# Optimization experiments

Hardware: AMD Instinct MI355X
Metric: run time of the kernel (lower is better)

The kernel has to match this reference:

```python
import jax, jax.numpy as jnp
import numpy as np

HID = 150

def _lstm_layer(x, Wih, Whh, bih, bhh):
    # x: [T, D] -> [T, HID]; PyTorch gate order i, f, g, o
    b = bih + bhh
    xg = x @ Wih.T + b  # precompute input contribution: [T, 4H]
    def step(carry, xg_t):
        h, c = carry
        g = xg_t + h @ Whh.T
        i, f, gg, o = jnp.split(g, 4)
        i = jax.nn.sigmoid(i); f = jax.nn.sigmoid(f)
        gg = jnp.tanh(gg); o = jax.nn.sigmoid(o)
        c = f * c + i * gg
        h = o * jnp.tanh(c)
        return (h, c), h
    init = (jnp.zeros((HID,), x.dtype), jnp.zeros((HID,), x.dtype))
    _, ys = jax.lax.scan(step, init, xg)
    return ys

def _bilstm(x, Wih, Whh, bih, bhh):
    # x: [T, D]; params stacked [L, 2, ...]
    out = x
    for l in range(Wih.shape[0]):
        fwd = _lstm_layer(out, Wih[l, 0], Whh[l, 0], bih[l, 0], bhh[l, 0])
        bwd = _lstm_layer(out[::-1], Wih[l, 1], Whh[l, 1], bih[l, 1], bhh[l, 1])[::-1]
        out = jnp.concatenate([fwd, bwd], axis=-1)  # [T, 2H]
    return out

def setup_inputs() -> dict:
    key = jax.random.key(0)
    ks = jax.random.split(key, 16)
    s = 0.1  # keep LSTM gates in a sane range
    return {
        "inputs_solv": jax.random.normal(ks[0], (1, 4096, 300), jnp.float32),
        "inputs_solu": jax.random.normal(ks[1], (1, 4096, 300), jnp.float32),
        "solv_Wih": jax.random.normal(ks[2], (2, 2, 600, 300), jnp.float32) * s,
        "solv_Whh": jax.random.normal(ks[3], (2, 2, 600, 150), jnp.float32) * s,
        "solv_bih": jax.random.normal(ks[4], (2, 2, 600), jnp.float32) * s,
        "solv_bhh": jax.random.normal(ks[5], (2, 2, 600), jnp.float32) * s,
        "solu_Wih": jax.random.normal(ks[6], (2, 2, 600, 300), jnp.float32) * s,
        "solu_Whh": jax.random.normal(ks[7], (2, 2, 600, 150), jnp.float32) * s,
        "solu_bih": jax.random.normal(ks[8], (2, 2, 600), jnp.float32) * s,
        "solu_bhh": jax.random.normal(ks[9], (2, 2, 600), jnp.float32) * s,
        "fc1_w": jax.random.normal(ks[10], (2000, 600), jnp.float32) * 0.02,
        "fc1_b": jax.random.normal(ks[11], (2000,), jnp.float32) * 0.02,
        "fc2_w": jax.random.normal(ks[12], (1, 2000), jnp.float32) * 0.02,
        "fc2_b": jax.random.normal(ks[13], (1,), jnp.float32) * 0.02,
    }

def reference(inputs_solv, inputs_solu, solv_Wih, solv_Whh, solv_bih, solv_bhh,
              solu_Wih, solu_Whh, solu_bih, solu_bhh, fc1_w, fc1_b, fc2_w, fc2_b):
    H = _bilstm(inputs_solv[0], solv_Wih, solv_Whh, solv_bih, solv_bhh)  # [Hs, 300]
    G = _bilstm(inputs_solu[0], solu_Wih, solu_Whh, solu_bih, solu_bhh)  # [Gs, 300]
    a_score = H @ G.T                      # fused version of the nested loop: [Hs, Gs]
    a = jax.nn.softmax(a_score, axis=1)
    P = a @ G                              # [Hs, 300]
    Q = a.T @ H                            # [Gs, 300]
    u = jnp.maximum(H, P)
    v = jnp.maximum(G, Q)
    inp = jnp.concatenate([u.sum(axis=0), v.sum(axis=0)], axis=0)  # [600]
    x = jax.nn.relu(inp @ fc1_w.T + fc1_b)
    return x @ fc2_w.T + fc2_b
```

## Files before the change

### kernel.cpp

```cpp
#include <hip/hip_runtime.h>
#include <hip/hip_fp16.h>
#include <cstddef>

#define T_LEN 4096
#define HID 150
#define G4 600
#define NC 300

typedef __attribute__((ext_vector_type(8))) short bf16x8;
typedef __attribute__((ext_vector_type(8))) _Float16 f16x8;
typedef __attribute__((ext_vector_type(4))) float f32x4;

__device__ __forceinline__ void barrier_lgkm() {
  asm volatile("s_waitcnt lgkmcnt(0)\n\ts_barrier" ::: "memory");
}

__device__ __forceinline__ float fsig(float x) {
  return __builtin_amdgcn_rcpf(1.f + __expf(-x));
}
__device__ __forceinline__ float ftanh(float x) {
  float ax = fabsf(x);
  float e = __expf(2.f * ax);
  float t = 1.f - 2.f * __builtin_amdgcn_rcpf(e + 1.f);
  return copysignf(t, x);
}
__device__ __forceinline__ unsigned short f2bf(float f) {
  unsigned u = __builtin_bit_cast(unsigned, f);
  u += 0x7fff + ((u >> 16) & 1);
  return (unsigned short)(u >> 16);
}

__global__ __launch_bounds__(512, 2) void lstm_scan(
    const float* __restrict__ whh_solv, const float* __restrict__ whh_solu,
    const float* __restrict__ xg_base,
    float* __restrict__ out_solv, float* __restrict__ out_solu, int layer)
{
  __shared__ __align__(16) unsigned short h_bf[160];
  __shared__ float g_s[640];
  const int c = blockIdx.x;
  const int net = c >> 1, dir = c & 1;
  const float* Whh = (net ? whh_solu : whh_solv) + (size_t)(layer * 2 + dir) * (G4 * HID);
  const float* xg = xg_base + (size_t)c * T_LEN * G4;
  float* out = (net ? out_solu : out_solv) + dir * HID;
  const int tid = threadIdx.x;
  const int lane = tid & 63, wv = tid >> 6;
  const int lrow = lane & 15, lq = lane >> 4;

  bf16x8 bfr[5][5];
#pragma unroll
  for (int j = 0; j < 5; j++) {
    const int jrow = 16 * (wv + 8 * j) + lrow;
#pragma unroll
    for (int kk = 0; kk < 5; kk++) {
      bf16x8 b;
#pragma unroll
      for (int i = 0; i < 8; i++) {
        const int k = kk * 32 + lq * 8 + i;
        const float v = (jrow < G4 && k < HID) ? Whh[(size_t)jrow * HID + k] : 0.f;
        b[i] = (short)f2bf(v);
      }
      bfr[j][kk] = b;
    }
  }
  if (tid < 160) h_bf[tid] = 0;
  float cst = 0.f;
  float xr0 = 0.f, xr1 = 0.f, xr2 = 0.f, xr3 = 0.f;
  if (tid < HID) {
    const int t0 = dir ? (T_LEN - 1) : 0;
    const float* xgr = xg + (size_t)t0 * G4 + tid;
    xr0 = xgr[0]; xr1 = xgr[HID]; xr2 = xgr[2 * HID]; xr3 = xgr[3 * HID];
  }
  bf16x8 af[5];
#pragma unroll
  for (int kk = 0; kk < 5; kk++) af[kk] = (bf16x8){0, 0, 0, 0, 0, 0, 0, 0};
  const f32x4 z4 = {0.f, 0.f, 0.f, 0.f};
  barrier_lgkm();

  for (int s = 0; s < T_LEN; s++) {
    const int t = dir ? (T_LEN - 1 - s) : s;
    if (lrow == 0) {
#pragma unroll
      for (int kk = 0; kk < 5; kk++) af[kk] = *(const bf16x8*)&h_bf[kk * 32 + lq * 8];
    }
    f32x4 acc[5];
#pragma unroll
    for (int j = 0; j < 5; j++)
      acc[j] = __builtin_amdgcn_mfma_f32_16x16x32_bf16(af[0], bfr[j][0], z4, 0, 0, 0);
#pragma unroll
    for (int kk = 1; kk < 5; kk++)
#pragma unroll
      for (int j = 0; j < 5; j++)
        acc[j] = __builtin_amdgcn_mfma_f32_16x16x32_bf16(af[kk], bfr[j][kk], acc[j], 0, 0, 0);
    if (lane < 16) {
#pragma unroll
      for (int j = 0; j < 5; j++) g_s[16 * (wv + 8 * j) + lane] = acc[j][0];
    }
    barrier_lgkm();
    if (tid < HID) {
      const int n = tid;
      float gi = xr0 + g_s[n];
      float gf = xr1 + g_s[HID + n];
      float gg = xr2 + g_s[2 * HID + n];
      float go = xr3 + g_s[3 * HID + n];
      if (s + 1 < T_LEN) {
        const int tn = dir ? (T_LEN - 2 - s) : (s + 1);
        const float* xgr = xg + (size_t)tn * G4 + n;
        xr0 = xgr[0]; xr1 = xgr[HID]; xr2 = xgr[2 * HID]; xr3 = xgr[3 * HID];
      }
      const float iv = fsig(gi), fv = fsig(gf), gv = ftanh(gg), ov = fsig(go);
      cst = fv * cst + iv * gv;
      const float hv = ov * ftanh(cst);
      h_bf[n] = f2bf(hv);
      out[(size_t)t * NC + n] = hv;
    }
    barrier_lgkm();
  }
}

__global__ void conv_w(const float* __restrict__ wv, const float* __restrict__ wu,
                       __half* __restrict__ dst)
{
  const int gid = blockIdx.x * 256 + threadIdx.x;
  if (gid >= 8 * 640 * 320) return;
  const int k = gid % 320, j = (gid / 320) % 640, s = gid / (320 * 640);
  const int l = s >> 2, net = (s >> 1) & 1, dir = s & 1;
  float v = 0.f;
  if (j < G4 && k < NC) {
    const float* src = (net ? wu : wv) + (size_t)(l * 2 + dir) * (G4 * NC);
    v = src[(size_t)j * NC + k];
  }
  dst[gid] = __float2half(v);
}

__global__ void conv_x(const float* __restrict__ src, __half* __restrict__ dst, int rows)
{
  const int gid = blockIdx.x * 256 + threadIdx.x;
  if (gid >= rows * 320) return;
  const int k = gid % 320, m = gid / 320;
  dst[gid] = __float2half(k < NC ? src[(size_t)m * NC + k] : 0.f);
}

__global__ void conv_t(const float* __restrict__ src, __half* __restrict__ dst)
{
  const int gid = blockIdx.x * 256 + threadIdx.x;
  if (gid >= 320 * 4096) return;
  const int m = gid % 4096, f = gid / 4096;
  dst[gid] = __float2half(f < NC ? src[(size_t)m * NC + f] : 0.f);
}

__global__ void zero_f(float* __restrict__ p, int n) {
  const int i = blockIdx.x * 256 + threadIdx.x;
  if (i < n) p[i] = 0.f;
}

__global__ __launch_bounds__(256) void xg_mfma(
    const __half* __restrict__ Av, const __half* __restrict__ Au,
    const __half* __restrict__ W,
    const float* __restrict__ bihv, const float* __restrict__ bhhv,
    const float* __restrict__ bihu, const float* __restrict__ bhhu,
    float* __restrict__ xg, int layer)
{
  const int tid = threadIdx.x;
  const int lane = tid & 63, wv = tid >> 6;
  const int ln = lane & 15, q = lane >> 4;
  const int chain = blockIdx.y;
  const __half* A = (chain >= 2) ? Au : Av;
  const __half* Wc = W + (size_t)chain * 640 * 320;
  const float* bi = ((chain >= 2) ? bihu : bihv) + (size_t)(layer * 2 + (chain & 1)) * G4;
  const float* bh = ((chain >= 2) ? bhhu : bhhv) + (size_t)(layer * 2 + (chain & 1)) * G4;
  float* C = xg + (size_t)chain * T_LEN * G4;
  const int m0 = blockIdx.x * 64 + wv * 16;
  const __half* Arow = A + (size_t)(m0 + ln) * 320;

  for (int nc = 0; nc < 4; nc++) {
    f32x4 acc[10];
#pragma unroll
    for (int j = 0; j < 10; j++) acc[j] = (f32x4){0.f, 0.f, 0.f, 0.f};
    for (int kk = 0; kk < 10; kk++) {
      const f16x8 afr = *(const f16x8*)(Arow + kk * 32 + q * 8);
#pragma unroll
      for (int j = 0; j < 10; j++) {
        const int n = nc * 160 + j * 16 + ln;
        const f16x8 bfr = *(const f16x8*)(Wc + (size_t)n * 320 + kk * 32 + q * 8);
        acc[j] = __builtin_amdgcn_mfma_f32_16x16x32_f16(afr, bfr, acc[j], 0, 0, 0);
      }
    }
#pragma unroll
    for (int j = 0; j < 10; j++) {
      const int n = nc * 160 + j * 16 + ln;
      if (n < G4) {
        const float bias = bi[n] + bh[n];
#pragma unroll
        for (int r = 0; r < 4; r++)
          C[(size_t)(m0 + q * 4 + r) * G4 + n] = acc[j][r] + bias;
      }
    }
  }
}

__global__ __launch_bounds__(256) void s_pass1(
    const __half* __restrict__ Hh, const __half* __restrict__ Gh,
    float* __restrict__ sums)
{
  const int tid = threadIdx.x;
  const int lane = tid & 63, wv = tid >> 6;
  const int ln = lane & 15, q = lane >> 4;
  const int m0 = blockIdx.x * 64 + wv * 16;
  const __half* Arow = Hh + (size_t)(m0 + ln) * 320;
  f16x8 afr[10];
#pragma unroll
  for (int kk = 0; kk < 10; kk++) afr[kk] = *(const f16x8*)(Arow + kk * 32 + q * 8);
  float rs[4] = {0.f, 0.f, 0.f, 0.f};
  const int nt0 = blockIdx.y * 64;
  for (int nt = 0; nt < 64; nt++) {
    const __half* Brow = Gh + (size_t)(16 * (nt0 + nt) + ln) * 320;
    f32x4 acc = (f32x4){0.f, 0.f, 0.f, 0.f};
#pragma unroll
    for (int kk = 0; kk < 10; kk++) {
      const f16x8 bfr = *(const f16x8*)(Brow + kk * 32 + q * 8);
      acc = __builtin_amdgcn_mfma_f32_16x16x32_f16(afr[kk], bfr, acc, 0, 0, 0);
    }
#pragma unroll
    for (int r = 0; r < 4; r++) rs[r] += __expf(fminf(acc[r] - 30.f, 80.f));
  }
#pragma unroll
  for (int m = 1; m <= 8; m <<= 1)
#pragma unroll
    for (int r = 0; r < 4; r++) rs[r] += __shfl_xor(rs[r], m);
  if (ln == 0) {
#pragma unroll
    for (int r = 0; r < 4; r++) atomicAdd(&sums[m0 + q * 4 + r], rs[r]);
  }
}

__global__ void invert_k(const float* __restrict__ sums, float* __restrict__ il) {
  const int i = blockIdx.x * 256 + threadIdx.x;
  if (i < 4096) il[i] = 1.f / sums[i];
}

__global__ __launch_bounds__(256) void s_pass2(
    const __half* __restrict__ Hh, const __half* __restrict__ Gh,
    const float* __restrict__ il, __half* __restrict__ AH)
{
  const int tid = threadIdx.x;
  const int lane = tid & 63, wv = tid >> 6;
  const int ln = lane & 15, q = lane >> 4;
  const int m0 = blockIdx.x * 64 + wv * 16;
  const __half* Arow = Hh + (size_t)(m0 + ln) * 320;
  f16x8 afr[10];
#pragma unroll
  for (int kk = 0; kk < 10; kk++) afr[kk] = *(const f16x8*)(Arow + kk * 32 + q * 8);
  float ilr[4];
#pragma unroll
  for (int r = 0; r < 4; r++) ilr[r] = il[m0 + q * 4 + r];
  const int nt0 = blockIdx.y * 64;
  for (int nt = 0; nt < 64; nt++) {
    const int n = 16 * (nt0 + nt) + ln;
    const __half* Brow = Gh + (size_t)n * 320;
    f32x4 acc = (f32x4){0.f, 0.f, 0.f, 0.f};
#pragma unroll
    for (int kk = 0; kk < 10; kk++) {
      const f16x8 bfr = *(const f16x8*)(Brow + kk * 32 + q * 8);
      acc = __builtin_amdgcn_mfma_f32_16x16x32_f16(afr[kk], bfr, acc, 0, 0, 0);
    }
#pragma unroll
    for (int r = 0; r < 4; r++) {
      const float a = __expf(fminf(acc[r] - 30.f, 80.f)) * ilr[r];
      AH[(size_t)(m0 + q * 4 + r) * 4096 + n] = __float2half(a);
    }
  }
}

__global__ __launch_bounds__(256) void p_mfma(
    const __half* __restrict__ AH, const __half* __restrict__ GhT,
    float* __restrict__ Pb)
{
  const int tid = threadIdx.x;
  const int lane = tid & 63, wv = tid >> 6;
  const int ln = lane & 15, q = lane >> 4;
  const int m0 = blockIdx.x * 64 + wv * 16;
  const __half* Arow = AH + (size_t)(m0 + ln) * 4096;

  for (int nc = 0; nc < 2; nc++) {
    f32x4 acc[10];
#pragma unroll
    for (int j = 0; j < 10; j++) acc[j] = (f32x4){0.f, 0.f, 0.f, 0.f};
    for (int kk = 0; kk < 128; kk++) {
      const f16x8 afr = *(const f16x8*)(Arow + kk * 32 + q * 8);
#pragma unroll
      for (int j = 0; j < 10; j++) {
        const int n = nc * 160 + j * 16 + ln;
        const f16x8 bfr = *(const f16x8*)(GhT + (size_t)n * 4096 + kk * 32 + q * 8);
        acc[j] = __builtin_amdgcn_mfma_f32_16x16x32_f16(afr, bfr, acc[j], 0, 0, 0);
      }
    }
#pragma unroll
    for (int j = 0; j < 10; j++) {
      const int n = nc * 160 + j * 16 + ln;
      if (n < NC) {
#pragma unroll
        for (int r = 0; r < 4; r++)
          Pb[(size_t)(m0 + q * 4 + r) * NC + n] = acc[j][r];
      }
    }
  }
}

__global__ __launch_bounds__(256) void qt_mfma(
    const __half* __restrict__ AH, const __half* __restrict__ HhT,
    float* __restrict__ Qb)
{
  __shared__ __align__(16) _Float16 Ats[64][72];
  const int tid = threadIdx.x;
  const int lane = tid & 63, wv = tid >> 6;
  const int ln = lane & 15, q = lane >> 4;
  const int j0 = blockIdx.x * 64;
  f32x4 acc[20];
#pragma unroll
  for (int j = 0; j < 20; j++) acc[j] = (f32x4){0.f, 0.f, 0.f, 0.f};
  const int il8 = tid >> 2, j8 = (tid & 3) * 16;

  for (int ic = 0; ic < 4096; ic += 64) {
    __syncthreads();
    {
      const __half* src = AH + (size_t)(ic + il8) * 4096 + j0 + j8;
      const f16x8 v0 = *(const f16x8*)src;
      const f16x8 v1 = *(const f16x8*)(src + 8);
#pragma unroll
      for (int jj = 0; jj < 8; jj++) Ats[j8 + jj][il8] = v0[jj];
#pragma unroll
      for (int jj = 0; jj < 8; jj++) Ats[j8 + 8 + jj][il8] = v1[jj];
    }
    __syncthreads();
#pragma unroll
    for (int s = 0; s < 2; s++) {
      const f16x8 afr = *(const f16x8*)&Ats[wv * 16 + ln][s * 32 + q * 8];
      const __half* bbase = HhT + ic + s * 32 + q * 8;
#pragma unroll
      for (int j = 0; j < 20; j++) {
        const f16x8 bfr = *(const f16x8*)(bbase + (size_t)(j * 16 + ln) * 4096);
        acc[j] = __builtin_amdgcn_mfma_f32_16x16x32_f16(afr, bfr, acc[j], 0, 0, 0);
      }
    }
  }
#pragma unroll
  for (int j = 0; j < 20; j++) {
    const int f = j * 16 + ln;
    if (f < NC) {
#pragma unroll
      for (int r = 0; r < 4; r++)
        Qb[(size_t)(j0 + wv * 16 + q * 4 + r) * NC + f] = acc[j][r];
    }
  }
}

__global__ void reduce_uv(const float* __restrict__ X, const float* __restrict__ Yp,
                          float* __restrict__ inp, int off)
{
  const int j = threadIdx.x;
  if (j >= NC) return;
  const int r0 = blockIdx.x * 128;
  float s = 0.f;
  for (int r = r0; r < r0 + 128; r++)
    s += fmaxf(X[(size_t)r * NC + j], Yp[(size_t)r * NC + j]);
  atomicAdd(&inp[off + j], s);
}

__global__ void fc1_k(const float* __restrict__ w1, const float* __restrict__ b1,
                      const float* __restrict__ inp, float* __restrict__ x)
{
  const int r = blockIdx.x * 256 + threadIdx.x;
  if (r >= 2000) return;
  float s = b1[r];
  const float* wr = w1 + (size_t)r * 600;
  for (int k = 0; k < 600; k++) s += wr[k] * inp[k];
  x[r] = fmaxf(s, 0.f);
}

__global__ void fc2_k(const float* __restrict__ x, const float* __restrict__ w2,
                      const float* __restrict__ b2, float* __restrict__ outp)
{
  const int tid = threadIdx.x;
  float s = 0.f;
  for (int i = tid; i < 2000; i += 256) s += x[i] * w2[i];
#pragma unroll
  for (int off = 32; off > 0; off >>= 1) s += __shfl_down(s, off);
  __shared__ float red[4];
  if ((tid & 63) == 0) red[tid >> 6] = s;
  __syncthreads();
  if (tid == 0) outp[0] = red[0] + red[1] + red[2] + red[3] + b2[0];
}

extern "C" void kernel_launch(void* const* d_in, const int* in_sizes, int n_in,
                              void* d_out, int out_size, void* d_ws, size_t ws_size,
                              hipStream_t stream)
{
  const float* in_solv  = (const float*)d_in[0];
  const float* in_solu  = (const float*)d_in[1];
  const float* solv_Wih = (const float*)d_in[2];
  const float* solv_Whh = (const float*)d_in[3];
  const float* solv_bih = (const float*)d_in[4];
  const float* solv_bhh = (const float*)d_in[5];
  const float* solu_Wih = (const float*)d_in[6];
  const float* solu_Whh = (const float*)d_in[7];
  const float* solu_bih = (const float*)d_in[8];
  const float* solu_bhh = (const float*)d_in[9];
  const float* fc1_w = (const float*)d_in[10];
  const float* fc1_b = (const float*)d_in[11];
  const float* fc2_w = (const float*)d_in[12];
  const float* fc2_b = (const float*)d_in[13];
  float* outp = (float*)d_out;
  float* ws = (float*)d_ws;

  constexpr size_t off_P   = 0;
  constexpr size_t off_Q   = 1228800;
  constexpr size_t off_inp = 2457600;
  constexpr size_t off_x   = 2458240;
  constexpr size_t off_il  = 2460288;
  constexpr size_t off_sm  = 2464384;
  constexpr size_t off_xg  = 2468480;
  constexpr size_t off_L0  = off_xg + (size_t)4 * 2457600;
  constexpr size_t off_HG  = off_L0 + (size_t)2 * 1228800;

  float*  xg   = ws + off_xg;
  float*  L0v  = ws + off_L0;
  float*  L0u  = L0v + 1228800;
  float*  Hb   = ws + off_HG;
  float*  Gb   = Hb + 1228800;
  float*  Pb   = ws + off_P;
  float*  Qb   = ws + off_Q;
  float*  inp  = ws + off_inp;
  float*  xf   = ws + off_x;
  float*  il   = ws + off_il;
  float*  sums = ws + off_sm;
  __half* Wihh = (__half*)(ws + off_P);
  __half* Avh  = (__half*)(ws + off_L0);
  __half* Auh  = Avh + 4096 * 320;
  __half* L0vh = (__half*)(ws + off_HG);
  __half* L0uh = L0vh + 4096 * 320;
  __half* Hh   = (__half*)(ws + off_L0);
  __half* Gh   = Hh + 4096 * 320;
  __half* AH   = (__half*)(ws + off_xg);
  __half* HhT  = AH + (size_t)4096 * 4096;
  __half* GhT  = HhT + 320 * 4096;

  conv_w<<<(8 * 640 * 320 + 255) / 256, 256, 0, stream>>>(solv_Wih, solu_Wih, Wihh);
  conv_x<<<(4096 * 320 + 255) / 256, 256, 0, stream>>>(in_solv, Avh, 4096);
  conv_x<<<(4096 * 320 + 255) / 256, 256, 0, stream>>>(in_solu, Auh, 4096);

  xg_mfma<<<dim3(64, 4), 256, 0, stream>>>(Avh, Auh, Wihh,
      solv_bih, solv_bhh, solu_bih, solu_bhh, xg, 0);
  lstm_scan<<<4, 512, 0, stream>>>(solv_Whh, solu_Whh, xg, L0v, L0u, 0);

  conv_x<<<(4096 * 320 + 255) / 256, 256, 0, stream>>>(L0v, L0vh, 4096);
  conv_x<<<(4096 * 320 + 255) / 256, 256, 0, stream>>>(L0u, L0uh, 4096);
  xg_mfma<<<dim3(64, 4), 256, 0, stream>>>(L0vh, L0uh, Wihh + (size_t)4 * 640 * 320,
      solv_bih, solv_bhh, solu_bih, solu_bhh, xg, 1);
  lstm_scan<<<4, 512, 0, stream>>>(solv_Whh, solu_Whh, xg, Hb, Gb, 1);

  conv_x<<<(4096 * 320 + 255) / 256, 256, 0, stream>>>(Hb, Hh, 4096);
  conv_x<<<(4096 * 320 + 255) / 256, 256, 0, stream>>>(Gb, Gh, 4096);
  conv_t<<<(320 * 4096 + 255) / 256, 256, 0, stream>>>(Hb, HhT);
  conv_t<<<(320 * 4096 + 255) / 256, 256, 0, stream>>>(Gb, GhT);
  zero_f<<<16, 256, 0, stream>>>(sums, 4096);
  s_pass1<<<dim3(64, 4), 256, 0, stream>>>(Hh, Gh, sums);
  invert_k<<<16, 256, 0, stream>>>(sums, il);
  s_pass2<<<dim3(64, 4), 256, 0, stream>>>(Hh, Gh, il, AH);
  p_mfma<<<64, 256, 0, stream>>>(AH, GhT, Pb);
  qt_mfma<<<64, 256, 0, stream>>>(AH, HhT, Qb);

  zero_f<<<3, 256, 0, stream>>>(inp, 640);
  reduce_uv<<<32, 320, 0, stream>>>(Hb, Pb, inp, 0);
  reduce_uv<<<32, 320, 0, stream>>>(Gb, Qb, inp, 300);
  fc1_k<<<8, 256, 0, stream>>>(fc1_w, fc1_b, inp, xf);
  fc2_k<<<1, 256, 0, stream>>>(xf, fc2_w, fc2_b, outp);
}
```

Measured before the change: 7.672 ms.

## Remap LSTM gate rows per wave to drop shared-memory gate exchange and a barrier

Recurrent weight rows are reassigned so that each wave's MFMA tiles produce all four gates for its own hidden units. Waves 0-7 cover units 0-127, and a fifth tile, run only by waves 0-5, carries units 128-149 with interleaved gates gathered by lane shuffles. This removes the g_s shared buffer and one of the two block barriers in each of the 4096 serial timesteps, and skips the padded MFMAs on the last two waves. The cost is that nothing separates one wave's read of h_bf from another wave's write of the new h within the same step, so correctness relies on timing rather than a barrier.

```diff
diff --git a/kernel.cpp b/kernel.cpp
--- a/kernel.cpp
+++ b/kernel.cpp
@@ -36,7 +36,6 @@
     float* __restrict__ out_solv, float* __restrict__ out_solu, int layer)
 {
   __shared__ __align__(16) unsigned short h_bf[160];
-  __shared__ float g_s[640];
   const int c = blockIdx.x;
   const int net = c >> 1, dir = c & 1;
   const float* Whh = (net ? whh_solu : whh_solv) + (size_t)(layer * 2 + dir) * (G4 * HID);
@@ -44,31 +43,40 @@
   float* out = (net ? out_solu : out_solv) + dir * HID;
   const int tid = threadIdx.x;
   const int lane = tid & 63, wv = tid >> 6;
-  const int lrow = lane & 15, lq = lane >> 4;
+  const int l = lane & 15, q = lane >> 4;
+  const int u = 16 * wv + l;
+  const bool gate_lane = (lane < 16);
+  const bool sec_lane = gate_lane && ((l & 3) == 0) && (u < 88);
+  const int cp = u;
+  const int cs = 128 + (u >> 2);
 
   bf16x8 bfr[5][5];
 #pragma unroll
   for (int j = 0; j < 5; j++) {
-    const int jrow = 16 * (wv + 8 * j) + lrow;
+    int row;
+    if (j < 4) row = j * HID + u;
+    else       row = (u < 88) ? (u & 3) * HID + 128 + (u >> 2) : -1;
 #pragma unroll
     for (int kk = 0; kk < 5; kk++) {
       bf16x8 b;
 #pragma unroll
       for (int i = 0; i < 8; i++) {
-        const int k = kk * 32 + lq * 8 + i;
-        const float v = (jrow < G4 && k < HID) ? Whh[(size_t)jrow * HID + k] : 0.f;
+        const int k = kk * 32 + q * 8 + i;
+        const float v = (row >= 0 && k < HID) ? Whh[(size_t)row * HID + k] : 0.f;
         b[i] = (short)f2bf(v);
       }
       bfr[j][kk] = b;
     }
   }
   if (tid < 160) h_bf[tid] = 0;
-  float cst = 0.f;
-  float xr0 = 0.f, xr1 = 0.f, xr2 = 0.f, xr3 = 0.f;
-  if (tid < HID) {
+  float cstp = 0.f, csts = 0.f;
+  float xp0 = 0.f, xp1 = 0.f, xp2 = 0.f, xp3 = 0.f;
+  float xs0 = 0.f, xs1 = 0.f, xs2 = 0.f, xs3 = 0.f;
+  {
     const int t0 = dir ? (T_LEN - 1) : 0;
-    const float* xgr = xg + (size_t)t0 * G4 + tid;
-    xr0 = xgr[0]; xr1 = xgr[HID]; xr2 = xgr[2 * HID]; xr3 = xgr[3 * HID];
+    const float* base = xg + (size_t)t0 * G4;
+    if (gate_lane) { xp0 = base[cp]; xp1 = base[HID + cp]; xp2 = base[2 * HID + cp]; xp3 = base[3 * HID + cp]; }
+    if (sec_lane)  { xs0 = base[cs]; xs1 = base[HID + cs]; xs2 = base[2 * HID + cs]; xs3 = base[3 * HID + cs]; }
   }
   bf16x8 af[5];
 #pragma unroll
@@ -78,40 +86,48 @@
 
   for (int s = 0; s < T_LEN; s++) {
     const int t = dir ? (T_LEN - 1 - s) : s;
-    if (lrow == 0) {
-#pragma unroll
-      for (int kk = 0; kk < 5; kk++) af[kk] = *(const bf16x8*)&h_bf[kk * 32 + lq * 8];
+    if (l == 0) {
+#pragma unroll
+      for (int kk = 0; kk < 5; kk++) af[kk] = *(const bf16x8*)&h_bf[kk * 32 + q * 8];
     }
     f32x4 acc[5];
 #pragma unroll
-    for (int j = 0; j < 5; j++)
+    for (int j = 0; j < 4; j++)
       acc[j] = __builtin_amdgcn_mfma_f32_16x16x32_bf16(af[0], bfr[j][0], z4, 0, 0, 0);
-#pragma unroll
-    for (int kk = 1; kk < 5; kk++)
-#pragma unroll
-      for (int j = 0; j < 5; j++)
+    if (wv < 6)
+      acc[4] = __builtin_amdgcn_mfma_f32_16x16x32_bf16(af[0], bfr[4][0], z4, 0, 0, 0);
+#pragma unroll
+    for (int kk = 1; kk < 5; kk++) {
+#pragma unroll
+      for (int j = 0; j < 4; j++)
         acc[j] = __builtin_amdgcn_mfma_f32_16x16x32_bf16(af[kk], bfr[j][kk], acc[j], 0, 0, 0);
-    if (lane < 16) {
-#pragma unroll
-      for (int j = 0; j < 5; j++) g_s[16 * (wv + 8 * j) + lane] = acc[j][0];
-    }
-    barrier_lgkm();
-    if (tid < HID) {
-      const int n = tid;
-      float gi = xr0 + g_s[n];
-      float gf = xr1 + g_s[HID + n];
-      float gg = xr2 + g_s[2 * HID + n];
-      float go = xr3 + g_s[3 * HID + n];
+      if (wv < 6)
+        acc[4] = __builtin_amdgcn_mfma_f32_16x16x32_bf16(af[kk], bfr[4][kk], acc[4], 0, 0, 0);
+    }
+    if (gate_lane) {
+      const float g4 = acc[4][0];
+      const int b4 = lane & ~3;
+      const float v0 = __shfl(g4, b4), v1 = __shfl(g4, b4 | 1);
+      const float v2 = __shfl(g4, b4 | 2), v3 = __shfl(g4, b4 | 3);
+      if (sec_lane) {
+        const float si = xs0 + v0, sf = xs1 + v1, sg = xs2 + v2, so = xs3 + v3;
+        csts = fsig(sf) * csts + fsig(si) * ftanh(sg);
+        const float hs = fsig(so) * ftanh(csts);
+        h_bf[cs] = f2bf(hs);
+        out[(size_t)t * NC + cs] = hs;
+      }
+      const float gi = xp0 + acc[0][0], gf = xp1 + acc[1][0];
+      const float gg = xp2 + acc[2][0], go = xp3 + acc[3][0];
+      cstp = fsig(gf) * cstp + fsig(gi) * ftanh(gg);
+      const float hp = fsig(go) * ftanh(cstp);
+      h_bf[cp] = f2bf(hp);
+      out[(size_t)t * NC + cp] = hp;
       if (s + 1 < T_LEN) {
         const int tn = dir ? (T_LEN - 2 - s) : (s + 1);
-        const float* xgr = xg + (size_t)tn * G4 + n;
-        xr0 = xgr[0]; xr1 = xgr[HID]; xr2 = xgr[2 * HID]; xr3 = xgr[3 * HID];
-      }
-      const float iv = fsig(gi), fv = fsig(gf), gv = ftanh(gg), ov = fsig(go);
-      cst = fv * cst + iv * gv;
-      const float hv = ov * ftanh(cst);
-      h_bf[n] = f2bf(hv);
-      out[(size_t)t * NC + n] = hv;
+        const float* base = xg + (size_t)tn * G4;
+        xp0 = base[cp]; xp1 = base[HID + cp]; xp2 = base[2 * HID + cp]; xp3 = base[3 * HID + cp];
+        if (sec_lane) { xs0 = base[cs]; xs1 = base[HID + cs]; xs2 = base[2 * HID + cs]; xs3 = base[3 * HID + cs]; }
+      }
     }
     barrier_lgkm();
   }
```

After: 9.483 ms. 23.6% more time.

## Regroup LSTM gate rows per wave and double-buffer h to drop a barrier

Applied to the files above, without the earlier changes.

The recurrent scan now assigns each of 10 waves the four gate rows (i,f,g,o) for the same 16 hidden units. Each wave can then compute the cell update directly from its MFMA accumulators instead of exchanging gate values through shared memory. The hidden state is double-buffered in LDS, so each timestep needs only one barrier instead of two. The cost is a larger block of 640 threads and some padded rows in the last wave.

```diff
diff --git a/kernel.cpp b/kernel.cpp
--- a/kernel.cpp
+++ b/kernel.cpp
@@ -30,13 +30,12 @@
   return (unsigned short)(u >> 16);
 }
 
-__global__ __launch_bounds__(512, 2) void lstm_scan(
+__global__ __launch_bounds__(640, 3) void lstm_scan(
     const float* __restrict__ whh_solv, const float* __restrict__ whh_solu,
     const float* __restrict__ xg_base,
     float* __restrict__ out_solv, float* __restrict__ out_solu, int layer)
 {
-  __shared__ __align__(16) unsigned short h_bf[160];
-  __shared__ float g_s[640];
+  __shared__ __align__(16) unsigned short hb[2][160];
   const int c = blockIdx.x;
   const int net = c >> 1, dir = c & 1;
   const float* Whh = (net ? whh_solu : whh_solv) + (size_t)(layer * 2 + dir) * (G4 * HID);
@@ -45,74 +44,75 @@
   const int tid = threadIdx.x;
   const int lane = tid & 63, wv = tid >> 6;
   const int lrow = lane & 15, lq = lane >> 4;
-
-  bf16x8 bfr[5][5];
-#pragma unroll
-  for (int j = 0; j < 5; j++) {
-    const int jrow = 16 * (wv + 8 * j) + lrow;
-#pragma unroll
-    for (int kk = 0; kk < 5; kk++) {
-      bf16x8 b;
-#pragma unroll
-      for (int i = 0; i < 8; i++) {
-        const int k = kk * 32 + lq * 8 + i;
-        const float v = (jrow < G4 && k < HID) ? Whh[(size_t)jrow * HID + k] : 0.f;
-        b[i] = (short)f2bf(v);
-      }
-      bfr[j][kk] = b;
-    }
-  }
-  if (tid < 160) h_bf[tid] = 0;
+  const bool gl = (lane < 16) && (16 * wv + lane < HID);
+  const int ch = 16 * wv + lane;
+
+  bf16x8 bfr[4][5];
+  {
+    const int cc = 16 * wv + lrow;
+    const bool cv = (cc < HID);
+#pragma unroll
+    for (int j = 0; j < 4; j++) {
+      const size_t row = (size_t)(j * HID + cc) * HID;
+#pragma unroll
+      for (int kk = 0; kk < 5; kk++) {
+        bf16x8 b;
+#pragma unroll
+        for (int i = 0; i < 8; i++) {
+          const int k = kk * 32 + lq * 8 + i;
+          const float v = (cv && k < HID) ? Whh[row + k] : 0.f;
+          b[i] = (short)f2bf(v);
+        }
+        bfr[j][kk] = b;
+      }
+    }
+  }
+  if (tid < 160) { hb[0][tid] = 0; hb[1][tid] = 0; }
   float cst = 0.f;
   float xr0 = 0.f, xr1 = 0.f, xr2 = 0.f, xr3 = 0.f;
-  if (tid < HID) {
+  if (gl) {
     const int t0 = dir ? (T_LEN - 1) : 0;
-    const float* xgr = xg + (size_t)t0 * G4 + tid;
+    const float* xgr = xg + (size_t)t0 * G4 + ch;
     xr0 = xgr[0]; xr1 = xgr[HID]; xr2 = xgr[2 * HID]; xr3 = xgr[3 * HID];
   }
-  bf16x8 af[5];
-#pragma unroll
-  for (int kk = 0; kk < 5; kk++) af[kk] = (bf16x8){0, 0, 0, 0, 0, 0, 0, 0};
   const f32x4 z4 = {0.f, 0.f, 0.f, 0.f};
   barrier_lgkm();
 
+  int p = 0;
   for (int s = 0; s < T_LEN; s++) {
     const int t = dir ? (T_LEN - 1 - s) : s;
-    if (lrow == 0) {
-#pragma unroll
-      for (int kk = 0; kk < 5; kk++) af[kk] = *(const bf16x8*)&h_bf[kk * 32 + lq * 8];
-    }
-    f32x4 acc[5];
-#pragma unroll
-    for (int j = 0; j < 5; j++)
+    bf16x8 af[5];
+#pragma unroll
+    for (int kk = 0; kk < 5; kk++) {
+      bf16x8 a = {0, 0, 0, 0, 0, 0, 0, 0};
+      if (lrow == 0) a = *(const bf16x8*)&hb[p][kk * 32 + lq * 8];
+      af[kk] = a;
+    }
+    f32x4 acc[4];
+#pragma unroll
+    for (int j = 0; j < 4; j++)
       acc[j] = __builtin_amdgcn_mfma_f32_16x16x32_bf16(af[0], bfr[j][0], z4, 0, 0, 0);
 #pragma unroll
     for (int kk = 1; kk < 5; kk++)
 #pragma unroll
-      for (int j = 0; j < 5; j++)
+      for (int j = 0; j < 4; j++)
         acc[j] = __builtin_amdgcn_mfma_f32_16x16x32_bf16(af[kk], bfr[j][kk], acc[j], 0, 0, 0);
-    if (lane < 16) {
-#pragma unroll
-      for (int j = 0; j < 5; j++) g_s[16 * (wv + 8 * j) + lane] = acc[j][0];
-    }
-    barrier_lgkm();
-    if (tid < HID) {
-      const int n = tid;
-      float gi = xr0 + g_s[n];
-      float gf = xr1 + g_s[HID + n];
-      float gg = xr2 + g_s[2 * HID + n];
-      float go = xr3 + g_s[3 * HID + n];
+    if (gl) {
+      const float gi = xr0 + acc[0][0];
+      const float gf = xr1 + acc[1][0];
+      const float gg = xr2 + acc[2][0];
+      const float go = xr3 + acc[3][0];
       if (s + 1 < T_LEN) {
         const int tn = dir ? (T_LEN - 2 - s) : (s + 1);
-        const float* xgr = xg + (size_t)tn * G4 + n;
+        const float* xgr = xg + (size_t)tn * G4 + ch;
         xr0 = xgr[0]; xr1 = xgr[HID]; xr2 = xgr[2 * HID]; xr3 = xgr[3 * HID];
       }
-      const float iv = fsig(gi), fv = fsig(gf), gv = ftanh(gg), ov = fsig(go);
-      cst = fv * cst + iv * gv;
-      const float hv = ov * ftanh(cst);
-      h_bf[n] = f2bf(hv);
-      out[(size_t)t * NC + n] = hv;
-    }
+      cst = fsig(gf) * cst + fsig(gi) * ftanh(gg);
+      const float hv = fsig(go) * ftanh(cst);
+      hb[1 - p][ch] = f2bf(hv);
+      out[(size_t)t * NC + ch] = hv;
+    }
+    p ^= 1;
     barrier_lgkm();
   }
 }
@@ -450,13 +450,13 @@
 
   xg_mfma<<<dim3(64, 4), 256, 0, stream>>>(Avh, Auh, Wihh,
       solv_bih, solv_bhh, solu_bih, solu_bhh, xg, 0);
-  lstm_scan<<<4, 512, 0, stream>>>(solv_Whh, solu_Whh, xg, L0v, L0u, 0);
+  lstm_scan<<<4, 640, 0, stream>>>(solv_Whh, solu_Whh, xg, L0v, L0u, 0);
 
   conv_x<<<(4096 * 320 + 255) / 256, 256, 0, stream>>>(L0v, L0vh, 4096);
   conv_x<<<(4096 * 320 + 255) / 256, 256, 0, stream>>>(L0u, L0uh, 4096);
   xg_mfma<<<dim3(64, 4), 256, 0, stream>>>(L0vh, L0uh, Wihh + (size_t)4 * 640 * 320,
       solv_bih, solv_bhh, solu_bih, solu_bhh, xg, 1);
-  lstm_scan<<<4, 512, 0, stream>>>(solv_Whh, solu_Whh, xg, Hb, Gb, 1);
+  lstm_scan<<<4, 640, 0, stream>>>(solv_Whh, solu_Whh, xg, Hb, Gb, 1);
 
   conv_x<<<(4096 * 320 + 255) / 256, 256, 0, stream>>>(Hb, Hh, 4096);
   conv_x<<<(4096 * 320 + 255) / 256, 256, 0, stream>>>(Gb, Gh, 4096);
```

Measured after the change: 7.784 ms. Within noise of the previous version (+1.5%).

## Emit fp16 LSTM outputs directly, compute attention scores once, merge P/Q GEMMs

Applied to the files above, without the earlier changes.

The LSTM scan now writes fp16 outputs straight into the padded layout the next stage reads, so the separate conv_x conversion launches go away. A zero pass over the padded buffer sets the unused columns. The two-pass softmax that recomputed H·G^T twice is replaced by one score GEMM that stores fp16 logits, followed by a row-sum kernel and an in-place exp/scale kernel. The P and Q^T GEMMs are merged into one launch of 128 blocks so they run concurrently. Storing raw logits in fp16 before the exponential adds rounding error, and the new approach reads and writes the 4096x4096 matrix several extra times.

```diff
diff --git a/kernel.cpp b/kernel.cpp
--- a/kernel.cpp
+++ b/kernel.cpp
@@ -33,7 +33,8 @@
 __global__ __launch_bounds__(512, 2) void lstm_scan(
     const float* __restrict__ whh_solv, const float* __restrict__ whh_solu,
     const float* __restrict__ xg_base,
-    float* __restrict__ out_solv, float* __restrict__ out_solu, int layer)
+    float* __restrict__ o32v, float* __restrict__ o32u,
+    __half* __restrict__ o16v, __half* __restrict__ o16u, int layer, int w32)
 {
   __shared__ __align__(16) unsigned short h_bf[160];
   __shared__ float g_s[640];
@@ -41,7 +42,8 @@
   const int net = c >> 1, dir = c & 1;
   const float* Whh = (net ? whh_solu : whh_solv) + (size_t)(layer * 2 + dir) * (G4 * HID);
   const float* xg = xg_base + (size_t)c * T_LEN * G4;
-  float* out = (net ? out_solu : out_solv) + dir * HID;
+  float* out32 = (net ? o32u : o32v) + dir * HID;
+  __half* out16 = (net ? o16u : o16v) + dir * HID;
   const int tid = threadIdx.x;
   const int lane = tid & 63, wv = tid >> 6;
   const int lrow = lane & 15, lq = lane >> 4;
@@ -70,24 +72,22 @@
     const float* xgr = xg + (size_t)t0 * G4 + tid;
     xr0 = xgr[0]; xr1 = xgr[HID]; xr2 = xgr[2 * HID]; xr3 = xgr[3 * HID];
   }
-  bf16x8 af[5];
-#pragma unroll
-  for (int kk = 0; kk < 5; kk++) af[kk] = (bf16x8){0, 0, 0, 0, 0, 0, 0, 0};
-  const f32x4 z4 = {0.f, 0.f, 0.f, 0.f};
   barrier_lgkm();
 
   for (int s = 0; s < T_LEN; s++) {
     const int t = dir ? (T_LEN - 1 - s) : s;
-    if (lrow == 0) {
-#pragma unroll
-      for (int kk = 0; kk < 5; kk++) af[kk] = *(const bf16x8*)&h_bf[kk * 32 + lq * 8];
+    bf16x8 af[5];
+#pragma unroll
+    for (int kk = 0; kk < 5; kk++) {
+      bf16x8 a = {0, 0, 0, 0, 0, 0, 0, 0};
+      if (lrow == 0) a = *(const bf16x8*)&h_bf[kk * 32 + lq * 8];
+      af[kk] = a;
     }
     f32x4 acc[5];
 #pragma unroll
-    for (int j = 0; j < 5; j++)
-      acc[j] = __builtin_amdgcn_mfma_f32_16x16x32_bf16(af[0], bfr[j][0], z4, 0, 0, 0);
-#pragma unroll
-    for (int kk = 1; kk < 5; kk++)
+    for (int j = 0; j < 5; j++) acc[j] = (f32x4){0.f, 0.f, 0.f, 0.f};
+#pragma unroll
+    for (int kk = 0; kk < 5; kk++)
 #pragma unroll
       for (int j = 0; j < 5; j++)
         acc[j] = __builtin_amdgcn_mfma_f32_16x16x32_bf16(af[kk], bfr[j][kk], acc[j], 0, 0, 0);
@@ -111,7 +111,8 @@
       cst = fv * cst + iv * gv;
       const float hv = ov * ftanh(cst);
       h_bf[n] = f2bf(hv);
-      out[(size_t)t * NC + n] = hv;
+      out16[(size_t)t * 320 + n] = __float2half(hv);
+      if (w32) out32[(size_t)t * NC + n] = hv;
     }
     barrier_lgkm();
   }
@@ -198,9 +199,9 @@
   }
 }
 
-__global__ __launch_bounds__(256) void s_pass1(
+__global__ __launch_bounds__(256) void s_gemm(
     const __half* __restrict__ Hh, const __half* __restrict__ Gh,
-    float* __restrict__ sums)
+    __half* __restrict__ AH)
 {
   const int tid = threadIdx.x;
   const int lane = tid & 63, wv = tid >> 6;
@@ -210,49 +211,6 @@
   f16x8 afr[10];
 #pragma unroll
   for (int kk = 0; kk < 10; kk++) afr[kk] = *(const f16x8*)(Arow + kk * 32 + q * 8);
-  float rs[4] = {0.f, 0.f, 0.f, 0.f};
-  const int nt0 = blockIdx.y * 64;
-  for (int nt = 0; nt < 64; nt++) {
-    const __half* Brow = Gh + (size_t)(16 * (nt0 + nt) + ln) * 320;
-    f32x4 acc = (f32x4){0.f, 0.f, 0.f, 0.f};
-#pragma unroll
-    for (int kk = 0; kk < 10; kk++) {
-      const f16x8 bfr = *(const f16x8*)(Brow + kk * 32 + q * 8);
-      acc = __builtin_amdgcn_mfma_f32_16x16x32_f16(afr[kk], bfr, acc, 0, 0, 0);
-    }
-#pragma unroll
-    for (int r = 0; r < 4; r++) rs[r] += __expf(fminf(acc[r] - 30.f, 80.f));
-  }
-#pragma unroll
-  for (int m = 1; m <= 8; m <<= 1)
-#pragma unroll
-    for (int r = 0; r < 4; r++) rs[r] += __shfl_xor(rs[r], m);
-  if (ln == 0) {
-#pragma unroll
-    for (int r = 0; r < 4; r++) atomicAdd(&sums[m0 + q * 4 + r], rs[r]);
-  }
-}
-
-__global__ void invert_k(const float* __restrict__ sums, float* __restrict__ il) {
-  const int i = blockIdx.x * 256 + threadIdx.x;
-  if (i < 4096) il[i] = 1.f / sums[i];
-}
-
-__global__ __launch_bounds__(256) void s_pass2(
-    const __half* __restrict__ Hh, const __half* __restrict__ Gh,
-    const float* __restrict__ il, __half* __restrict__ AH)
-{
-  const int tid = threadIdx.x;
-  const int lane = tid & 63, wv = tid >> 6;
-  const int ln = lane & 15, q = lane >> 4;
-  const int m0 = blockIdx.x * 64 + wv * 16;
-  const __half* Arow = Hh + (size_t)(m0 + ln) * 320;
-  f16x8 afr[10];
-#pragma unroll
-  for (int kk = 0; kk < 10; kk++) afr[kk] = *(const f16x8*)(Arow + kk * 32 + q * 8);
-  float ilr[4];
-#pragma unroll
-  for (int r = 0; r < 4; r++) ilr[r] = il[m0 + q * 4 + r];
   const int nt0 = blockIdx.y * 64;
   for (int nt = 0; nt < 64; nt++) {
     const int n = 16 * (nt0 + nt) + ln;
@@ -264,92 +222,116 @@
       acc = __builtin_amdgcn_mfma_f32_16x16x32_f16(afr[kk], bfr, acc, 0, 0, 0);
     }
 #pragma unroll
-    for (int r = 0; r < 4; r++) {
-      const float a = __expf(fminf(acc[r] - 30.f, 80.f)) * ilr[r];
-      AH[(size_t)(m0 + q * 4 + r) * 4096 + n] = __float2half(a);
-    }
-  }
-}
-
-__global__ __launch_bounds__(256) void p_mfma(
+    for (int r = 0; r < 4; r++)
+      AH[(size_t)(m0 + q * 4 + r) * 4096 + n] = __float2half(acc[r]);
+  }
+}
+
+__global__ __launch_bounds__(256) void rowsum_k(const __half* __restrict__ AH,
+                                                float* __restrict__ il)
+{
+  const int m = blockIdx.x, tid = threadIdx.x;
+  const __half* row = AH + (size_t)m * 4096;
+  float s = 0.f;
+  for (int i = tid * 8; i < 4096; i += 2048) {
+    const f16x8 v = *(const f16x8*)(row + i);
+#pragma unroll
+    for (int j = 0; j < 8; j++) s += __expf(fminf((float)v[j] - 30.f, 80.f));
+  }
+#pragma unroll
+  for (int off = 32; off > 0; off >>= 1) s += __shfl_down(s, off);
+  __shared__ float red[4];
+  if ((tid & 63) == 0) red[tid >> 6] = s;
+  __syncthreads();
+  if (tid == 0) il[m] = 1.f / (red[0] + red[1] + red[2] + red[3]);
+}
+
+__global__ __launch_bounds__(256) void scale_k(__half* __restrict__ AH,
+                                               const float* __restrict__ il)
+{
+  const size_t gid = (size_t)blockIdx.x * 256 + threadIdx.x;
+  const int m = (int)(gid >> 9);
+  const float ilm = il[m];
+  f16x8 v = *(f16x8*)(AH + gid * 8);
+#pragma unroll
+  for (int j = 0; j < 8; j++)
+    v[j] = (_Float16)(__expf(fminf((float)v[j] - 30.f, 80.f)) * ilm);
+  *(f16x8*)(AH + gid * 8) = v;
+}
+
+__global__ __launch_bounds__(256) void pq_mfma(
     const __half* __restrict__ AH, const __half* __restrict__ GhT,
-    float* __restrict__ Pb)
-{
-  const int tid = threadIdx.x;
-  const int lane = tid & 63, wv = tid >> 6;
-  const int ln = lane & 15, q = lane >> 4;
-  const int m0 = blockIdx.x * 64 + wv * 16;
-  const __half* Arow = AH + (size_t)(m0 + ln) * 4096;
-
-  for (int nc = 0; nc < 2; nc++) {
-    f32x4 acc[10];
-#pragma unroll
-    for (int j = 0; j < 10; j++) acc[j] = (f32x4){0.f, 0.f, 0.f, 0.f};
-    for (int kk = 0; kk < 128; kk++) {
-      const f16x8 afr = *(const f16x8*)(Arow + kk * 32 + q * 8);
-#pragma unroll
-      for (int j = 0; j < 10; j++) {
-        const int n = nc * 160 + j * 16 + ln;
-        const f16x8 bfr = *(const f16x8*)(GhT + (size_t)n * 4096 + kk * 32 + q * 8);
-        acc[j] = __builtin_amdgcn_mfma_f32_16x16x32_f16(afr, bfr, acc[j], 0, 0, 0);
-      }
-    }
-#pragma unroll
-    for (int j = 0; j < 10; j++) {
-      const int n = nc * 160 + j * 16 + ln;
-      if (n < NC) {
-#pragma unroll
-        for (int r = 0; r < 4; r++)
-          Pb[(size_t)(m0 + q * 4 + r) * NC + n] = acc[j][r];
-      }
-    }
-  }
-}
-
-__global__ __launch_bounds__(256) void qt_mfma(
-    const __half* __restrict__ AH, const __half* __restrict__ HhT,
-    float* __restrict__ Qb)
+    const __half* __restrict__ HhT,
+    float* __restrict__ Pb, float* __restrict__ Qb)
 {
   __shared__ __align__(16) _Float16 Ats[64][72];
   const int tid = threadIdx.x;
   const int lane = tid & 63, wv = tid >> 6;
   const int ln = lane & 15, q = lane >> 4;
-  const int j0 = blockIdx.x * 64;
-  f32x4 acc[20];
-#pragma unroll
-  for (int j = 0; j < 20; j++) acc[j] = (f32x4){0.f, 0.f, 0.f, 0.f};
-  const int il8 = tid >> 2, j8 = (tid & 3) * 16;
-
-  for (int ic = 0; ic < 4096; ic += 64) {
-    __syncthreads();
-    {
-      const __half* src = AH + (size_t)(ic + il8) * 4096 + j0 + j8;
-      const f16x8 v0 = *(const f16x8*)src;
-      const f16x8 v1 = *(const f16x8*)(src + 8);
-#pragma unroll
-      for (int jj = 0; jj < 8; jj++) Ats[j8 + jj][il8] = v0[jj];
-#pragma unroll
-      for (int jj = 0; jj < 8; jj++) Ats[j8 + 8 + jj][il8] = v1[jj];
-    }
-    __syncthreads();
-#pragma unroll
-    for (int s = 0; s < 2; s++) {
-      const f16x8 afr = *(const f16x8*)&Ats[wv * 16 + ln][s * 32 + q * 8];
-      const __half* bbase = HhT + ic + s * 32 + q * 8;
-#pragma unroll
-      for (int j = 0; j < 20; j++) {
-        const f16x8 bfr = *(const f16x8*)(bbase + (size_t)(j * 16 + ln) * 4096);
-        acc[j] = __builtin_amdgcn_mfma_f32_16x16x32_f16(afr, bfr, acc[j], 0, 0, 0);
-      }
-    }
-  }
-#pragma unroll
-  for (int j = 0; j < 20; j++) {
-    const int f = j * 16 + ln;
-    if (f < NC) {
-#pragma unroll
-      for (int r = 0; r < 4; r++)
-        Qb[(size_t)(j0 + wv * 16 + q * 4 + r) * NC + f] = acc[j][r];
+
+  if (blockIdx.x < 64) {
+    const int m0 = blockIdx.x * 64 + wv * 16;
+    const __half* Arow = AH + (size_t)(m0 + ln) * 4096;
+    for (int nc = 0; nc < 2; nc++) {
+      f32x4 acc[10];
+#pragma unroll
+      for (int j = 0; j < 10; j++) acc[j] = (f32x4){0.f, 0.f, 0.f, 0.f};
+      for (int kk = 0; kk < 128; kk++) {
+        const f16x8 afr = *(const f16x8*)(Arow + kk * 32 + q * 8);
+#pragma unroll
+        for (int j = 0; j < 10; j++) {
+          const int n = nc * 160 + j * 16 + ln;
+          const f16x8 bfr = *(const f16x8*)(GhT + (size_t)n * 4096 + kk * 32 + q * 8);
+          acc[j] = __builtin_amdgcn_mfma_f32_16x16x32_f16(afr, bfr, acc[j], 0, 0, 0);
+        }
+      }
+#pragma unroll
+      for (int j = 0; j < 10; j++) {
+        const int n = nc * 160 + j * 16 + ln;
+        if (n < NC) {
+#pragma unroll
+          for (int r = 0; r < 4; r++)
+            Pb[(size_t)(m0 + q * 4 + r) * NC + n] = acc[j][r];
+        }
+      }
+    }
+  } else {
+    const int j0 = (blockIdx.x - 64) * 64;
+    f32x4 acc[20];
+#pragma unroll
+    for (int j = 0; j < 20; j++) acc[j] = (f32x4){0.f, 0.f, 0.f, 0.f};
+    const int il8 = tid >> 2, j8 = (tid & 3) * 16;
+    for (int ic = 0; ic < 4096; ic += 64) {
+      __syncthreads();
+      {
+        const __half* src = AH + (size_t)(ic + il8) * 4096 + j0 + j8;
+        const f16x8 v0 = *(const f16x8*)src;
+        const f16x8 v1 = *(const f16x8*)(src + 8);
+#pragma unroll
+        for (int jj = 0; jj < 8; jj++) Ats[j8 + jj][il8] = v0[jj];
+#pragma unroll
+        for (int jj = 0; jj < 8; jj++) Ats[j8 + 8 + jj][il8] = v1[jj];
+      }
+      __syncthreads();
+#pragma unroll
+      for (int s = 0; s < 2; s++) {
+        const f16x8 afr = *(const f16x8*)&Ats[wv * 16 + ln][s * 32 + q * 8];
+        const __half* bbase = HhT + ic + s * 32 + q * 8;
+#pragma unroll
+        for (int j = 0; j < 20; j++) {
+          const f16x8 bfr = *(const f16x8*)(bbase + (size_t)(j * 16 + ln) * 4096);
+          acc[j] = __builtin_amdgcn_mfma_f32_16x16x32_f16(afr, bfr, acc[j], 0, 0, 0);
+        }
+      }
+    }
+#pragma unroll
+    for (int j = 0; j < 20; j++) {
+      const int f = j * 16 + ln;
+      if (f < NC) {
+#pragma unroll
+        for (int r = 0; r < 4; r++)
+          Qb[(size_t)(j0 + wv * 16 + q * 4 + r) * NC + f] = acc[j][r];
+      }
     }
   }
 }
@@ -417,14 +399,11 @@
   constexpr size_t off_inp = 2457600;
   constexpr size_t off_x   = 2458240;
   constexpr size_t off_il  = 2460288;
-  constexpr size_t off_sm  = 2464384;
   constexpr size_t off_xg  = 2468480;
   constexpr size_t off_L0  = off_xg + (size_t)4 * 2457600;
-  constexpr size_t off_HG  = off_L0 + (size_t)2 * 1228800;
+  constexpr size_t off_HG  = off_L0 + 1310720;
 
   float*  xg   = ws + off_xg;
-  float*  L0v  = ws + off_L0;
-  float*  L0u  = L0v + 1228800;
   float*  Hb   = ws + off_HG;
   float*  Gb   = Hb + 1228800;
   float*  Pb   = ws + off_P;
@@ -432,7 +411,6 @@
   float*  inp  = ws + off_inp;
   float*  xf   = ws + off_x;
   float*  il   = ws + off_il;
-  float*  sums = ws + off_sm;
   __half* Wihh = (__half*)(ws + off_P);
   __half* Avh  = (__half*)(ws + off_L0);
   __half* Auh  = Avh + 4096 * 320;
@@ -444,30 +422,27 @@
   __half* HhT  = AH + (size_t)4096 * 4096;
   __half* GhT  = HhT + 320 * 4096;
 
+  zero_f<<<5120, 256, 0, stream>>>(ws + off_HG, 1310720);
   conv_w<<<(8 * 640 * 320 + 255) / 256, 256, 0, stream>>>(solv_Wih, solu_Wih, Wihh);
-  conv_x<<<(4096 * 320 + 255) / 256, 256, 0, stream>>>(in_solv, Avh, 4096);
-  conv_x<<<(4096 * 320 + 255) / 256, 256, 0, stream>>>(in_solu, Auh, 4096);
+  conv_x<<<5120, 256, 0, stream>>>(in_solv, Avh, 4096);
+  conv_x<<<5120, 256, 0, stream>>>(in_solu, Auh, 4096);
 
   xg_mfma<<<dim3(64, 4), 256, 0, stream>>>(Avh, Auh, Wihh,
       solv_bih, solv_bhh, solu_bih, solu_bhh, xg, 0);
-  lstm_scan<<<4, 512, 0, stream>>>(solv_Whh, solu_Whh, xg, L0v, L0u, 0);
-
-  conv_x<<<(4096 * 320 + 255) / 256, 256, 0, stream>>>(L0v, L0vh, 4096);
-  conv_x<<<(4096 * 320 + 255) / 256, 256, 0, stream>>>(L0u, L0uh, 4096);
+  lstm_scan<<<4, 512, 0, stream>>>(solv_Whh, solu_Whh, xg,
+      nullptr, nullptr, L0vh, L0uh, 0, 0);
+
   xg_mfma<<<dim3(64, 4), 256, 0, stream>>>(L0vh, L0uh, Wihh + (size_t)4 * 640 * 320,
       solv_bih, solv_bhh, solu_bih, solu_bhh, xg, 1);
-  lstm_scan<<<4, 512, 0, stream>>>(solv_Whh, solu_Whh, xg, Hb, Gb, 1);
-
-  conv_x<<<(4096 * 320 + 255) / 256, 256, 0, stream>>>(Hb, Hh, 4096);
-  conv_x<<<(4096 * 320 + 255) / 256, 256, 0, stream>>>(Gb, Gh, 4096);
-  conv_t<<<(320 * 4096 + 255) / 256, 256, 0, stream>>>(Hb, HhT);
-  conv_t<<<(320 * 4096 + 255) / 256, 256, 0, stream>>>(Gb, GhT);
-  zero_f<<<16, 256, 0, stream>>>(sums, 4096);
-  s_pass1<<<dim3(64, 4), 256, 0, stream>>>(Hh, Gh, sums);
-  invert_k<<<16, 256, 0, stream>>>(sums, il);
-  s_pass2<<<dim3(64, 4), 256, 0, stream>>>(Hh, Gh, il, AH);
-  p_mfma<<<64, 256, 0, stream>>>(AH, GhT, Pb);
-  qt_mfma<<<64, 256, 0, stream>>>(AH, HhT, Qb);
+  lstm_scan<<<4, 512, 0, stream>>>(solv_Whh, solu_Whh, xg,
+      Hb, Gb, Hh, Gh, 1, 1);
+
+  conv_t<<<5120, 256, 0, stream>>>(Hb, HhT);
+  conv_t<<<5120, 256, 0, stream>>>(Gb, GhT);
+  s_gemm<<<dim3(64, 4), 256, 0, stream>>>(Hh, Gh, AH);
+  rowsum_k<<<4096, 256, 0, stream>>>(AH, il);
+  scale_k<<<8192, 256, 0, stream>>>(AH, il);
+  pq_mfma<<<128, 256, 0, stream>>>(AH, GhT, HhT, Pb, Qb);
 
   zero_f<<<3, 256, 0, stream>>>(inp, 640);
   reduce_uv<<<32, 320, 0, stream>>>(Hb, Pb, inp, 0);
```

Result: faster. 7.064 ms, median of 2 (-7.9%).
